# Performance work log

Hardware: AMD Instinct MI355X
Metric: run time of the kernel (lower is better)

The kernel has to match this reference:

```python
import jax, jax.numpy as jnp
import numpy as np


def setup_inputs() -> dict:
    key = jax.random.key(0)
    B, N, D = 4, 8192, 16
    inputs = jax.random.normal(key, (B, N, D), dtype=jnp.float32)
    return {"inputs": inputs, "k": 16}


def reference(inputs, k):
    # pairwise squared distances: ||x_i||^2 - 2 x_i.x_j + ||x_j||^2  -> [B, N, N]
    inner = -2.0 * jnp.einsum("bnd,bmd->bnm", inputs, inputs)
    square = jnp.sum(inputs * inputs, axis=-1, keepdims=True)  # [B, N, 1]
    adj = square + inner + jnp.swapaxes(square, 1, 2)          # [B, N, N]
    # k smallest distances -> top-k of negated matrix
    _, nn_idx = jax.lax.top_k(-adj, k)                          # [B, N, k]
    return nn_idx
```

## Files before the change

kernel.cpp:

```cpp
#include <hip/hip_runtime.h>


#define B_    4
#define N_    8192
#define D_    16
#define K_    16
#define SEGS_ 8
#define SEG_  (N_ / SEGS_)
#define CH_   8
#define NCH_  (SEG_ / CH_)
#define BT_   512
#define CAP_  12
#define NQ_   (B_ * N_)

typedef unsigned long long u64;

__device__ __forceinline__ float np_norm16(const float* __restrict__ p) {
#pragma clang fp contract(off)
  float m[16];
#pragma unroll
  for (int d = 0; d < 16; ++d) m[d] = p[d] * p[d];
  float r[8];
#pragma unroll
  for (int j = 0; j < 8; ++j) r[j] = m[j] + m[j + 8];
  float q[4];
#pragma unroll
  for (int j = 0; j < 4; ++j) q[j] = r[j] + r[j + 4];
  return (q[0] + q[2]) + (q[1] + q[3]);
}

__device__ __forceinline__ unsigned mono32(float f) {
  unsigned u = __float_as_uint(f);
  return u ^ ((unsigned)((int)u >> 31) | 0x80000000u);
}

__global__ __launch_bounds__(256) void knn_norms(const float* __restrict__ x,
                                                 float* __restrict__ nrm) {
  int q = blockIdx.x * 256 + threadIdx.x;
  float row[16];
  const float4* xv = (const float4*)(x + (size_t)q * D_);
  float4 a = xv[0], b = xv[1], c = xv[2], d = xv[3];
  row[0]=a.x; row[1]=a.y; row[2]=a.z; row[3]=a.w;
  row[4]=b.x; row[5]=b.y; row[6]=b.z; row[7]=b.w;
  row[8]=c.x; row[9]=c.y; row[10]=c.z; row[11]=c.w;
  row[12]=d.x; row[13]=d.y; row[14]=d.z; row[15]=d.w;
  nrm[q] = np_norm16(row);
}

__device__ __forceinline__ void insert16(float d, int j, float (&kd)[K_], int (&ki)[K_]) {
  float cd = d; int ci = j;
#pragma unroll
  for (int p = 0; p < K_; ++p) {
    bool gt = kd[p] > cd;
    float t0 = gt ? cd : kd[p];
    float t1 = gt ? kd[p] : cd;
    int   t2 = gt ? ci : ki[p];
    int   t3 = gt ? ki[p] : ci;
    kd[p] = t0; cd = t1; ki[p] = t2; ci = t3;
  }
}

__device__ __forceinline__ void flushbuf(u64* __restrict__ pbuf, int tid,
                                         int& count, float& thr,
                                         float (&kd)[K_], int (&ki)[K_]) {
#pragma unroll 1
  for (int s = 0; s < CAP_; ++s) {
    if (s < count) {
      u64 e = pbuf[(size_t)s * BT_ + tid];
      float d = __uint_as_float((unsigned)(e >> 32));
      if (d < thr) {
        int j = (int)(e & 0xffffu);
        insert16(d, j, kd, ki);
        thr = kd[K_ - 1];
      }
    }
  }
  count = 0;
}

__global__ __launch_bounds__(BT_, 2) void knn_fused(const float* __restrict__ x,
                                                    const float* __restrict__ nrm,
                                                    int* __restrict__ out) {
  __shared__ u64 smem[8192];
  float4* stageR = (float4*)smem;
  float*  stageN = (float*)(smem + 1024);
  u64*    pbuf   = smem + 1088;

  const int tid  = threadIdx.x;
  const int w    = tid >> 6;
  const int lane = tid & 63;
  const int q    = blockIdx.x * 64 + lane;
  const int bq   = (int)((blockIdx.x * 64u) >> 13);
  const int row0 = bq * N_ + w * SEG_;
  const float* __restrict__ cbase = x + (size_t)row0 * D_;
  const float* __restrict__ nbase = nrm + row0;

  float qa[D_];
  {
    const float4* qv = (const float4*)(x + (size_t)q * D_);
    float4 v0 = qv[0], v1 = qv[1], v2 = qv[2], v3 = qv[3];
    qa[0]=v0.x; qa[1]=v0.y; qa[2]=v0.z; qa[3]=v0.w;
    qa[4]=v1.x; qa[5]=v1.y; qa[6]=v1.z; qa[7]=v1.w;
    qa[8]=v2.x; qa[9]=v2.y; qa[10]=v2.z; qa[11]=v2.w;
    qa[12]=v3.x; qa[13]=v3.y; qa[14]=v3.z; qa[15]=v3.w;
  }
  const float ni = nrm[q];

  float kd[K_]; int ki[K_];
#pragma unroll
  for (int p = 0; p < K_; ++p) { kd[p] = 3.4e38f; ki[p] = 0; }
  float thr = 3.4e38f;
  int count = 0;

  {
    const float4* gs = (const float4*)cbase;
    if (lane < 32) stageR[(w * 2 + 0) * 32 + lane] = gs[lane];
    if (lane < CH_) stageN[(w * 2 + 0) * CH_ + lane] = nbase[lane];
  }

#pragma unroll 1
  for (int c = 0; c < NCH_; ++c) {
    const int b = c & 1;
    float4 p0; float pn = 0.f;
    const bool more = (c + 1 < NCH_);
    if (more) {
      const float4* gs = (const float4*)(cbase + (size_t)(c + 1) * CH_ * D_);
      if (lane < 32) p0 = gs[lane];
      if (lane < CH_) pn = nbase[(c + 1) * CH_ + lane];
    }

    const float4* rows = stageR + (w * 2 + b) * 32;
    const float*  nn   = stageN + (w * 2 + b) * CH_;

#pragma unroll 1
    for (int t = 0; t < CH_; t += 2) {
      float4 r00 = rows[t*4+0], r01 = rows[t*4+1], r02 = rows[t*4+2], r03 = rows[t*4+3];
      float4 r10 = rows[t*4+4], r11 = rows[t*4+5], r12 = rows[t*4+6], r13 = rows[t*4+7];
      float nj0 = nn[t], nj1 = nn[t + 1];

      float c0[16] = {r00.x,r00.y,r00.z,r00.w, r01.x,r01.y,r01.z,r01.w,
                      r02.x,r02.y,r02.z,r02.w, r03.x,r03.y,r03.z,r03.w};
      float c1[16] = {r10.x,r10.y,r10.z,r10.w, r11.x,r11.y,r11.z,r11.w,
                      r12.x,r12.y,r12.z,r12.w, r13.x,r13.y,r13.z,r13.w};

      float dot0 = 0.f, dot1 = 0.f;
#pragma unroll
      for (int d = 0; d < D_; ++d) {
        dot0 = __builtin_fmaf(qa[d], c0[d], dot0);
        dot1 = __builtin_fmaf(qa[d], c1[d], dot1);
      }
      float d0, d1;
      {
#pragma clang fp contract(off)
        float i0 = -2.0f * dot0;  float i1 = -2.0f * dot1;
        float u0 = ni + i0;       float u1 = ni + i1;
        d0 = u0 + nj0;            d1 = u1 + nj1;
      }

      if (d0 < thr) {
        pbuf[(size_t)count * BT_ + tid] =
            ((u64)__float_as_uint(d0) << 32) | (unsigned)(c * CH_ + t);
        ++count;
      }
      if (d1 < thr) {
        pbuf[(size_t)count * BT_ + tid] =
            ((u64)__float_as_uint(d1) << 32) | (unsigned)(c * CH_ + t + 1);
        ++count;
      }
      if (__any(count >= CAP_ - 1)) flushbuf(pbuf, tid, count, thr, kd, ki);
    }

    if (more) {
      if (lane < 32) stageR[(w * 2 + (b ^ 1)) * 32 + lane] = p0;
      if (lane < CH_) stageN[(w * 2 + (b ^ 1)) * CH_ + lane] = pn;
    }
  }
  flushbuf(pbuf, tid, count, thr, kd, ki);

  __syncthreads();
#pragma unroll
  for (int p = 0; p < K_; ++p) {
    smem[((size_t)w * 16 + p) * 64 + lane] =
        ((u64)mono32(kd[p]) << 32) | (unsigned)(w * SEG_ + ki[p]);
  }
  __syncthreads();

  {
    const int qi = w * 8 + (lane >> 3);
    const int s  = lane & 7;
    const int gq = blockIdx.x * 64 + qi;
    int ptr = 0;
#pragma unroll 1
    for (int r = 0; r < K_; ++r) {
      u64 h = smem[((size_t)s * 16 + ptr) * 64 + qi];
      u64 m = h, o;
      o = __shfl_xor(m, 1); m = (o < m) ? o : m;
      o = __shfl_xor(m, 2); m = (o < m) ? o : m;
      o = __shfl_xor(m, 4); m = (o < m) ? o : m;
      if (h == m) ++ptr;
      if (s == 0) out[(size_t)gq * K_ + r] = (int)(m & 0xffffu);
    }
  }
}

extern "C" void kernel_launch(void* const* d_in, const int* in_sizes, int n_in,
                              void* d_out, int out_size, void* d_ws, size_t ws_size,
                              hipStream_t stream) {
  const float* x = (const float*)d_in[0];
  float* nrm = (float*)d_ws;
  int* out = (int*)d_out;

  knn_norms<<<NQ_ / 256, 256, 0, stream>>>(x, nrm);
  knn_fused<<<NQ_ / 64, BT_, 0, stream>>>(x, nrm, out);
}
```

Before: 329.4 us.

## Shrink LDS footprint and split final merge in halves to raise occupancy

Cuts the shared-memory allocation from 64KB to about 48KB by lowering the per-thread candidate buffer capacity and reusing the buffer region for a two-pass final merge over half the queries at a time. The launch bounds hint goes from 2 to 6 waves per SIMD, so more blocks can be resident per CU and memory and LDS latency can be hidden better. In exchange, flushes happen more often, the merge gains extra barriers with half the threads idle, and the register cap may force spills.

```diff
diff --git a/kernel.cpp b/kernel.cpp
--- a/kernel.cpp
+++ b/kernel.cpp
@@ -10,7 +10,7 @@
 #define CH_   8
 #define NCH_  (SEG_ / CH_)
 #define BT_   512
-#define CAP_  12
+#define CAP_  10
 #define NQ_   (B_ * N_)
 
 typedef unsigned long long u64;
@@ -78,10 +78,10 @@
   count = 0;
 }
 
-__global__ __launch_bounds__(BT_, 2) void knn_fused(const float* __restrict__ x,
+__global__ __launch_bounds__(BT_, 6) void knn_fused(const float* __restrict__ x,
                                                     const float* __restrict__ nrm,
                                                     int* __restrict__ out) {
-  __shared__ u64 smem[8192];
+  __shared__ u64 smem[6208];
   float4* stageR = (float4*)smem;
   float*  stageN = (float*)(smem + 1024);
   u64*    pbuf   = smem + 1088;
@@ -177,29 +177,40 @@
   }
   flushbuf(pbuf, tid, count, thr, kd, ki);
 
+  u64* mrg = smem + 1088;
+  const int half = lane >> 5;
+  const int lm   = lane & 31;
+
   __syncthreads();
-#pragma unroll
-  for (int p = 0; p < K_; ++p) {
-    smem[((size_t)w * 16 + p) * 64 + lane] =
-        ((u64)mono32(kd[p]) << 32) | (unsigned)(w * SEG_ + ki[p]);
-  }
-  __syncthreads();
-
-  {
-    const int qi = w * 8 + (lane >> 3);
-    const int s  = lane & 7;
-    const int gq = blockIdx.x * 64 + qi;
-    int ptr = 0;
-#pragma unroll 1
-    for (int r = 0; r < K_; ++r) {
-      u64 h = smem[((size_t)s * 16 + ptr) * 64 + qi];
-      u64 m = h, o;
-      o = __shfl_xor(m, 1); m = (o < m) ? o : m;
-      o = __shfl_xor(m, 2); m = (o < m) ? o : m;
-      o = __shfl_xor(m, 4); m = (o < m) ? o : m;
-      if (h == m) ++ptr;
-      if (s == 0) out[(size_t)gq * K_ + r] = (int)(m & 0xffffu);
-    }
+#pragma unroll 1
+  for (int h = 0; h < 2; ++h) {
+    if (half == h) {
+#pragma unroll
+      for (int p = 0; p < K_; ++p) {
+        mrg[((size_t)w * 16 + p) * 32 + lm] =
+            ((u64)mono32(kd[p]) << 32) | (unsigned)(w * SEG_ + ki[p]);
+      }
+    }
+    __syncthreads();
+
+    if (tid < 256) {
+      const int m  = tid >> 3;
+      const int s  = tid & 7;
+      const int qi = h * 32 + m;
+      const int gq = blockIdx.x * 64 + qi;
+      int ptr = 0;
+#pragma unroll 1
+      for (int r = 0; r < K_; ++r) {
+        u64 hd = mrg[((size_t)s * 16 + ptr) * 32 + m];
+        u64 mv = hd, o;
+        o = __shfl_xor(mv, 1); mv = (o < mv) ? o : mv;
+        o = __shfl_xor(mv, 2); mv = (o < mv) ? o : mv;
+        o = __shfl_xor(mv, 4); mv = (o < mv) ? o : mv;
+        if (hd == mv) ++ptr;
+        if (s == 0) out[(size_t)gq * K_ + r] = (int)(mv & 0xffffu);
+      }
+    }
+    __syncthreads();
   }
 }
 
```

New measurement: 1.158 ms. +251.7%, slower.
